# Kernel tuning notes

Hardware: AMD Instinct MI355X
Metric: run time of the kernel (lower is better)

## Reference

```python
import jax, jax.numpy as jnp
import numpy as np

HIDDEN = 1024
HEADS = 16
HEAD_DIM = HIDDEN // HEADS  # 64
LOCAL = (128, 128)
ROPE_MAX_POS = LOCAL[0] + LOCAL[1]  # 256 (local attention branch)
ROPE_BASE = 10000.0


def make_rope_cache(max_len, dim, base):
    positions = jnp.arange(max_len, dtype=jnp.float32)
    theta = 1.0 / base ** (jnp.arange(0, dim, 2, dtype=jnp.float32) / dim)
    angles = jnp.einsum('i,j->ij', positions, theta)
    return jnp.stack([jnp.cos(angles), jnp.sin(angles)], axis=-1)  # (max_len, dim//2, 2)


def apply_rope(x, cache):
    # x: (B, S, H, D); cache: (max_pos, D//2, 2)
    S = x.shape[1]
    pos = jnp.arange(S) % cache.shape[0]
    rc = cache[pos][None, :, None, :, :]  # (1, S, 1, D//2, 2)
    xr = x.reshape(*x.shape[:-1], -1, 2)
    x0, x1 = xr[..., 0], xr[..., 1]
    c, s = rc[..., 0], rc[..., 1]
    out = jnp.stack([x0 * c - x1 * s, x1 * c + x0 * s], axis=-1)
    return out.reshape(x.shape)


def sliding_window_mask(S, window, dtype):
    rel = jnp.arange(S)[:, None] - jnp.arange(S)[None, :]
    inside = (rel >= -window[0]) & (rel <= window[1])
    return jnp.where(inside, jnp.zeros((), dtype), -jnp.inf)[None, None]  # (1,1,S,S)


def setup_inputs() -> dict:
    key = jax.random.key(0)
    k1, k2, k3, k4, k5 = jax.random.split(key, 5)
    B, S = 2, 2048
    hidden_states = jax.random.normal(k1, (B, S, HIDDEN), dtype=jnp.float32)
    Wqkv_kernel = jax.random.normal(k2, (HIDDEN, 3 * HIDDEN), dtype=jnp.float32) / np.sqrt(HIDDEN)
    Wqkv_bias = jnp.zeros((3 * HIDDEN,), dtype=jnp.float32)
    Wo_kernel = jax.random.normal(k3, (HIDDEN, HIDDEN), dtype=jnp.float32) / np.sqrt(HIDDEN)
    Wo_bias = jnp.zeros((HIDDEN,), dtype=jnp.float32)
    rope_cache = make_rope_cache(ROPE_MAX_POS, HEAD_DIM, ROPE_BASE)
    return {
        'hidden_states': hidden_states,
        'Wqkv_kernel': Wqkv_kernel,
        'Wqkv_bias': Wqkv_bias,
        'Wo_kernel': Wo_kernel,
        'Wo_bias': Wo_bias,
        'rope_cache': rope_cache,
    }


def reference(hidden_states, Wqkv_kernel, Wqkv_bias, Wo_kernel, Wo_bias, rope_cache):
    B, S, _ = hidden_states.shape
    qkv = hidden_states @ Wqkv_kernel + Wqkv_bias  # (B,S,3*HIDDEN)
    qkv = qkv.reshape(B, S, 3, HEADS, HEAD_DIM)
    q = qkv[:, :, 0]  # (B,S,H,D)
    k = qkv[:, :, 1]
    v = qkv[:, :, 2]
    q = apply_rope(q, rope_cache)
    k = apply_rope(k, rope_cache)
    # to (B,H,S,D)
    q = jnp.transpose(q, (0, 2, 1, 3))
    k = jnp.transpose(k, (0, 2, 1, 3))
    v = jnp.transpose(v, (0, 2, 1, 3))
    scale = jnp.sqrt(jnp.float32(HEAD_DIM))
    scores = jnp.einsum('bhqd,bhkd->bhqk', q, k) / scale
    mask = sliding_window_mask(S, LOCAL, scores.dtype)
    probs = jax.nn.softmax(scores + mask, axis=-1)
    out = jnp.einsum('bhqk,bhkd->bqhd', probs, v).reshape(B, S, HIDDEN)
    out = out @ Wo_kernel + Wo_bias
    return out
```

## Files before the change

### kernel.cpp

```cpp
#include <hip/hip_runtime.h>
#include <hip/hip_bf16.h>

typedef __bf16 bf16x8 __attribute__((ext_vector_type(8)));
typedef __bf16 bf16x4 __attribute__((ext_vector_type(4)));
typedef float f32x4 __attribute__((ext_vector_type(4)));

#define SLEN 2048
#define NHEADS 16
#define HDIM 64

__global__ __launch_bounds__(256) void prep(const float* __restrict__ hidden,
                                            const float* __restrict__ Wqkv,
                                            const float* __restrict__ Wo,
                                            __bf16* __restrict__ A1,
                                            __bf16* __restrict__ Wt,
                                            __bf16* __restrict__ Wot) {
    int b = blockIdx.x;
    if (b < 4096) {
        int i = b * 256 + threadIdx.x;
        float4 v = reinterpret_cast<const float4*>(hidden)[i];
        bf16x4 o = { (__bf16)v.x, (__bf16)v.y, (__bf16)v.z, (__bf16)v.w };
        reinterpret_cast<bf16x4*>(A1)[i] = o;
        return;
    }
    __shared__ float tile[32][33];
    const float* W; __bf16* Dst; int N, n0, kc, bx, wn, j0, JNv;
    if (b < 7168) {
        int bb = b - 4096;
        int bx96 = bb % 96; kc = bb / 96;
        W = Wqkv; Dst = Wt; N = 3072;
        n0 = bx96 * 32;
        bx = bx96 >> 2; wn = (bx96 >> 1) & 1; j0 = (bx96 & 1) * 2; JNv = 4;
    } else {
        int bb = b - 7168;
        int bx32 = bb % 32; kc = bb / 32;
        W = Wo; Dst = Wot; N = 1024;
        n0 = bx32 * 32;
        bx = bx32 >> 1; wn = bx32 & 1; j0 = 0; JNv = 2;
    }
    int k0 = kc * 32;
    int tx = threadIdx.x & 31, ty = threadIdx.x >> 5;
    #pragma unroll
    for (int i = ty; i < 32; i += 8)
        tile[i][tx] = W[(size_t)(k0 + i) * N + n0 + tx];
    __syncthreads();
    if (threadIdx.x < 128) {
        int jh = threadIdx.x >> 6;
        int lane = threadIdx.x & 63;
        int lrow = lane & 15, quad = lane >> 4;
        bf16x8 val;
        #pragma unroll
        for (int i = 0; i < 8; i++)
            val[i] = (__bf16)tile[quad * 8 + i][jh * 16 + lrow];
        size_t idx = ((((size_t)(bx * 32 + kc) * 2 + wn) * JNv + (j0 + jh)) * 64 + lane);
        *reinterpret_cast<bf16x8*>(Dst + idx * 8) = val;
    }
}

template <int TN>
__global__ __launch_bounds__(256) void gemm_bt(const __bf16* __restrict__ A,
                                               const __bf16* __restrict__ Bfrag,
                                               const float* __restrict__ bias,
                                               float* __restrict__ Cf,
                                               __bf16* __restrict__ Cq,
                                               __bf16* __restrict__ Ck,
                                               __bf16* __restrict__ Cv,
                                               int M, int N, int K, int epi) {
    constexpr int JN = TN / 32;
    __shared__ __align__(16) __bf16 As[128 * 40];

    int nb = N / TN;
    int bx = blockIdx.x % nb;
    int by = blockIdx.x / nb;
    int row0 = by * 128, col0 = bx * TN;

    int tid = threadIdx.x;
    int wave = tid >> 6, lane = tid & 63;
    int quad = lane >> 4, lrow = lane & 15;
    int wm = wave >> 1, wn = wave & 1;

    int r1 = tid >> 2;
    int kk = (tid & 3) * 8;
    const __bf16* Aptr = A + (size_t)(row0 + r1) * K + kk;

    const __bf16* Bbase = Bfrag + ((size_t)(bx * 32) * 2 + wn) * JN * 512 + (size_t)lane * 8;

    f32x4 acc[4][JN];
    f32x4 zero = {0.f, 0.f, 0.f, 0.f};
    #pragma unroll
    for (int i = 0; i < 4; i++)
        #pragma unroll
        for (int j = 0; j < JN; j++) acc[i][j] = zero;

    int nkc = K >> 5;
    for (int kc = 0; kc < nkc; kc++) {
        int k0 = kc * 32;
        bf16x8 a0 = *reinterpret_cast<const bf16x8*>(Aptr + k0);
        bf16x8 a1 = *reinterpret_cast<const bf16x8*>(Aptr + (size_t)64 * K + k0);
        bf16x8 bfr[JN];
        #pragma unroll
        for (int j = 0; j < JN; j++)
            bfr[j] = *reinterpret_cast<const bf16x8*>(Bbase + (size_t)kc * JN * 1024 + j * 512);
        __syncthreads();
        *reinterpret_cast<bf16x8*>(&As[r1 * 40 + kk]) = a0;
        *reinterpret_cast<bf16x8*>(&As[(r1 + 64) * 40 + kk]) = a1;
        __syncthreads();

        bf16x8 af[4];
        #pragma unroll
        for (int i = 0; i < 4; i++)
            af[i] = *reinterpret_cast<const bf16x8*>(&As[(wm * 64 + i * 16 + lrow) * 40 + quad * 8]);
        #pragma unroll
        for (int i = 0; i < 4; i++)
            #pragma unroll
            for (int j = 0; j < JN; j++)
                acc[i][j] = __builtin_amdgcn_mfma_f32_16x16x32_bf16(af[i], bfr[j], acc[i][j], 0, 0, 0);
    }

    int part = col0 >> 10;
    #pragma unroll
    for (int i = 0; i < 4; i++) {
        int rowb = row0 + wm * 64 + i * 16 + quad * 4;
        #pragma unroll
        for (int j = 0; j < JN; j++) {
            int col = col0 + wn * (TN / 2) + j * 16 + lrow;
            float bsv = bias[col];
            #pragma unroll
            for (int r = 0; r < 4; r++) {
                int row = rowb + r;
                float v = acc[i][j][r] + bsv;
                if (epi == 0) {
                    Cf[(size_t)row * N + col] = v;
                } else {
                    int h = (col >> 6) & 15;
                    int d = col & 63;
                    int b = row >> 11;
                    int s = row & 2047;
                    __bf16* dst = (part == 0) ? Cq : ((part == 1) ? Ck : Cv);
                    dst[((size_t)(b * NHEADS + h) * SLEN + s) * HDIM + d] = (__bf16)v;
                }
            }
        }
    }
}

__device__ __forceinline__ bf16x8 rope8(bf16x8 v, f32x4 a, f32x4 b) {
    bf16x8 o;
    float e, od;
    e = (float)v[0]; od = (float)v[1];
    o[0] = (__bf16)(e * a[0] - od * a[1]); o[1] = (__bf16)(od * a[0] + e * a[1]);
    e = (float)v[2]; od = (float)v[3];
    o[2] = (__bf16)(e * a[2] - od * a[3]); o[3] = (__bf16)(od * a[2] + e * a[3]);
    e = (float)v[4]; od = (float)v[5];
    o[4] = (__bf16)(e * b[0] - od * b[1]); o[5] = (__bf16)(od * b[0] + e * b[1]);
    e = (float)v[6]; od = (float)v[7];
    o[6] = (__bf16)(e * b[2] - od * b[3]); o[7] = (__bf16)(od * b[2] + e * b[3]);
    return o;
}

__global__ __launch_bounds__(256) void rope_kernel(__bf16* __restrict__ Q,
                                                   __bf16* __restrict__ K,
                                                   const float* __restrict__ rope) {
    int idx = blockIdx.x * 256 + threadIdx.x;
    int chunk = idx & 7;
    int s = (idx >> 3) & 2047;
    int bh = idx >> 14;
    size_t off = ((size_t)bh * SLEN + s) * HDIM + chunk * 8;
    int pos = s & 255;
    const float* rp = rope + (size_t)pos * 64 + chunk * 8;
    f32x4 a = *reinterpret_cast<const f32x4*>(rp);
    f32x4 b = *reinterpret_cast<const f32x4*>(rp + 4);
    bf16x8 qv = *reinterpret_cast<bf16x8*>(Q + off);
    *reinterpret_cast<bf16x8*>(Q + off) = rope8(qv, a, b);
    bf16x8 kv = *reinterpret_cast<bf16x8*>(K + off);
    *reinterpret_cast<bf16x8*>(K + off) = rope8(kv, a, b);
}

__global__ __launch_bounds__(256) void attn_kernel(const __bf16* __restrict__ Q,
                                                   const __bf16* __restrict__ K,
                                                   const __bf16* __restrict__ V,
                                                   __bf16* __restrict__ O) {
    __shared__ __align__(16) __bf16 Vt[64][328];
    __shared__ __align__(16) __bf16 Pl[4][16][80];

    int qt = blockIdx.x & 31;
    int bh = blockIdx.x >> 5;
    int q0 = qt * 64;
    int kbase0 = q0 - 128;
    const __bf16* Qbh = Q + (size_t)bh * SLEN * HDIM;
    const __bf16* Kbh = K + (size_t)bh * SLEN * HDIM;
    const __bf16* Vbh = V + (size_t)bh * SLEN * HDIM;

    int tid = threadIdx.x;
    int wave = tid >> 6, lane = tid & 63;
    int quad = lane >> 4, lrow = lane & 15;
    int wq0 = q0 + wave * 16;

    {
        int dchunk = wave * 16;
        #pragma unroll
        for (int k = 0; k < 5; k++) {
            int off = k * 64 + lane;
            int krow = kbase0 + off;
            krow = min(max(krow, 0), SLEN - 1);
            const __bf16* vp = Vbh + (size_t)krow * HDIM + dchunk;
            bf16x8 v0 = *reinterpret_cast<const bf16x8*>(vp);
            bf16x8 v1 = *reinterpret_cast<const bf16x8*>(vp + 8);
            #pragma unroll
            for (int i = 0; i < 8; i++) {
                Vt[dchunk + i][off] = v0[i];
                Vt[dchunk + 8 + i][off] = v1[i];
            }
        }
    }

    bf16x8 qb0 = *reinterpret_cast<const bf16x8*>(Qbh + (size_t)(wq0 + lrow) * HDIM + quad * 8);
    bf16x8 qb1 = *reinterpret_cast<const bf16x8*>(Qbh + (size_t)(wq0 + lrow) * HDIM + 32 + quad * 8);

    __syncthreads();

    f32x4 zero = {0.f, 0.f, 0.f, 0.f};
    f32x4 acc[4], acc_l = zero;
    #pragma unroll
    for (int t = 0; t < 4; t++) acc[t] = zero;

    bf16x8 ones = { (__bf16)1.f, (__bf16)1.f, (__bf16)1.f, (__bf16)1.f,
                    (__bf16)1.f, (__bf16)1.f, (__bf16)1.f, (__bf16)1.f };

    int cbeg = wave >> 1;
    if (q0 < 128) { int e = (128 - q0) >> 5; if (e > cbeg) cbeg = e; }
    int cend = (16 * wave + 271) >> 5;
    { int e = (2175 - q0) >> 5; if (e < cend) cend = e; }

    auto loadK = [&](int c, bf16x8 (&kf)[2][2]) {
        int kb = kbase0 + c * 32;
        #pragma unroll
        for (int sub = 0; sub < 2; sub++) {
            int kr = kb + sub * 16 + lrow;
            int krc = min(max(kr, 0), SLEN - 1);
            const __bf16* kp = Kbh + (size_t)krc * HDIM;
            kf[sub][0] = *reinterpret_cast<const bf16x8*>(kp + quad * 8);
            kf[sub][1] = *reinterpret_cast<const bf16x8*>(kp + 32 + quad * 8);
        }
    };

    auto qkExp = [&](int c, bf16x8 (&kf)[2][2], int slot) {
        int kb = kbase0 + c * 32;
        int q = wq0 + lrow;
        #pragma unroll
        for (int sub = 0; sub < 2; sub++) {
            f32x4 st = __builtin_amdgcn_mfma_f32_16x16x32_bf16(kf[sub][0], qb0, zero, 0, 0, 0);
            st = __builtin_amdgcn_mfma_f32_16x16x32_bf16(kf[sub][1], qb1, st, 0, 0, 0);
            bf16x4 pk;
            #pragma unroll
            for (int r = 0; r < 4; r++) {
                int key = kb + sub * 16 + quad * 4 + r;
                int rel = key - q;
                bool valid = (rel >= -128) && (rel <= 128) && (key >= 0) && (key < SLEN);
                pk[r] = (__bf16)(valid ? __expf(st[r] * 0.125f) : 0.0f);
            }
            *reinterpret_cast<bf16x4*>(&Pl[wave][lrow][slot * 40 + sub * 16 + quad * 4]) = pk;
        }
    };

    auto pv = [&](int c, int slot) {
        int loc = c * 32;
        bf16x8 bp = *reinterpret_cast<const bf16x8*>(&Pl[wave][lrow][slot * 40 + quad * 8]);
        acc_l = __builtin_amdgcn_mfma_f32_16x16x32_bf16(ones, bp, acc_l, 0, 0, 0);
        #pragma unroll
        for (int t = 0; t < 4; t++) {
            bf16x8 va = *reinterpret_cast<const bf16x8*>(&Vt[t * 16 + lrow][loc + quad * 8]);
            acc[t] = __builtin_amdgcn_mfma_f32_16x16x32_bf16(va, bp, acc[t], 0, 0, 0);
        }
    };

    bf16x8 ka0[2][2], ka1[2][2];
    loadK(cbeg, ka0);
    loadK(cbeg + 1, ka1);
    int c = cbeg;
    while (c + 1 <= cend) {
        bf16x8 kn0[2][2], kn1[2][2];
        loadK(c + 2, kn0);
        loadK(c + 3, kn1);
        qkExp(c, ka0, 0);
        qkExp(c + 1, ka1, 1);
        asm volatile("s_waitcnt lgkmcnt(0)" ::: "memory");
        pv(c, 0);
        pv(c + 1, 1);
        #pragma unroll
        for (int sub = 0; sub < 2; sub++) {
            ka0[sub][0] = kn0[sub][0]; ka0[sub][1] = kn0[sub][1];
            ka1[sub][0] = kn1[sub][0]; ka1[sub][1] = kn1[sub][1];
        }
        c += 2;
    }
    if (c <= cend) {
        qkExp(c, ka0, 0);
        asm volatile("s_waitcnt lgkmcnt(0)" ::: "memory");
        pv(c, 0);
    }

    float inv = 1.0f / acc_l[0];
    int b = bh >> 4, h = bh & 15;
    int q = wq0 + lrow;
    size_t base = ((size_t)b * SLEN + q) * 1024 + h * HDIM;
    #pragma unroll
    for (int t = 0; t < 4; t++) {
        bf16x4 o;
        #pragma unroll
        for (int r = 0; r < 4; r++) o[r] = (__bf16)(acc[t][r] * inv);
        *reinterpret_cast<bf16x4*>(&O[base + t * 16 + quad * 4]) = o;
    }
}

extern "C" void kernel_launch(void* const* d_in, const int* in_sizes, int n_in,
                              void* d_out, int out_size, void* d_ws, size_t ws_size,
                              hipStream_t stream) {
    const float* hidden = (const float*)d_in[0];
    const float* Wqkv   = (const float*)d_in[1];
    const float* bqkv   = (const float*)d_in[2];
    const float* Wo     = (const float*)d_in[3];
    const float* bo     = (const float*)d_in[4];
    const float* rope   = (const float*)d_in[5];
    float* out = (float*)d_out;

    char* ws = (char*)d_ws;
    __bf16* A1  = (__bf16*)(ws);
    __bf16* Wt  = (__bf16*)(ws + 8388608);
    __bf16* Wot = (__bf16*)(ws + 14680064);
    __bf16* Qb  = (__bf16*)(ws + 16777216);
    __bf16* Kb  = (__bf16*)(ws + 25165824);
    __bf16* Vb  = (__bf16*)(ws + 33554432);
    __bf16* AO  = (__bf16*)(ws + 41943040);

    prep<<<8192, 256, 0, stream>>>(hidden, Wqkv, Wo, A1, Wt, Wot);

    gemm_bt<128><<<32 * 24, 256, 0, stream>>>(A1, Wt, bqkv, nullptr, Qb, Kb, Vb,
                                              4096, 3072, 1024, 1);
    rope_kernel<<<2048, 256, 0, stream>>>(Qb, Kb, rope);
    attn_kernel<<<1024, 256, 0, stream>>>(Qb, Kb, Vb, AO);
    gemm_bt<64><<<32 * 16, 256, 0, stream>>>(AO, Wot, bo, out, nullptr, nullptr, nullptr,
                                             4096, 1024, 1024, 0);
}
```

Before: 182.1 us.

## Pre-swizzle activations into MFMA fragment layout and use LDS-free QKV GEMM

```diff
diff --git a/kernel.cpp b/kernel.cpp
--- a/kernel.cpp
+++ b/kernel.cpp
@@ -16,37 +16,59 @@
                                             __bf16* __restrict__ Wt,
                                             __bf16* __restrict__ Wot) {
     int b = blockIdx.x;
-    if (b < 4096) {
-        int i = b * 256 + threadIdx.x;
-        float4 v = reinterpret_cast<const float4*>(hidden)[i];
-        bf16x4 o = { (__bf16)v.x, (__bf16)v.y, (__bf16)v.z, (__bf16)v.w };
-        reinterpret_cast<bf16x4*>(A1)[i] = o;
+    int t = threadIdx.x;
+    if (b < 1024) {
+        __shared__ float tile[128][33];
+        int by = b >> 5, kc = b & 31;
+        const float* src = hidden + (size_t)(by * 128) * 1024 + kc * 32;
+        #pragma unroll
+        for (int it = 0; it < 4; it++) {
+            int linear = it * 256 + t;
+            int r = linear >> 3, c4 = (linear & 7) * 4;
+            float4 v = *reinterpret_cast<const float4*>(src + (size_t)r * 1024 + c4);
+            tile[r][c4] = v.x; tile[r][c4 + 1] = v.y;
+            tile[r][c4 + 2] = v.z; tile[r][c4 + 3] = v.w;
+        }
+        __syncthreads();
+        int lane = t & 63, g = t >> 6;
+        int lrow = lane & 15, quad = lane >> 4;
+        #pragma unroll
+        for (int h = 0; h < 2; h++) {
+            int gg = g + h * 4;
+            int wm = gg >> 2, i = gg & 3;
+            int r = wm * 64 + i * 16 + lrow, c = quad * 8;
+            bf16x8 val;
+            #pragma unroll
+            for (int e = 0; e < 8; e++) val[e] = (__bf16)tile[r][c + e];
+            size_t off = ((size_t)by * 32 + kc) * 4096 + wm * 2048 + (size_t)i * 512 + (size_t)lane * 8;
+            *reinterpret_cast<bf16x8*>(A1 + off) = val;
+        }
         return;
     }
     __shared__ float tile[32][33];
     const float* W; __bf16* Dst; int N, n0, kc, bx, wn, j0, JNv;
-    if (b < 7168) {
-        int bb = b - 4096;
+    if (b < 4096) {
+        int bb = b - 1024;
         int bx96 = bb % 96; kc = bb / 96;
         W = Wqkv; Dst = Wt; N = 3072;
         n0 = bx96 * 32;
         bx = bx96 >> 2; wn = (bx96 >> 1) & 1; j0 = (bx96 & 1) * 2; JNv = 4;
     } else {
-        int bb = b - 7168;
+        int bb = b - 4096;
         int bx32 = bb % 32; kc = bb / 32;
         W = Wo; Dst = Wot; N = 1024;
         n0 = bx32 * 32;
         bx = bx32 >> 1; wn = bx32 & 1; j0 = 0; JNv = 2;
     }
     int k0 = kc * 32;
-    int tx = threadIdx.x & 31, ty = threadIdx.x >> 5;
+    int tx = t & 31, ty = t >> 5;
     #pragma unroll
     for (int i = ty; i < 32; i += 8)
         tile[i][tx] = W[(size_t)(k0 + i) * N + n0 + tx];
     __syncthreads();
-    if (threadIdx.x < 128) {
-        int jh = threadIdx.x >> 6;
-        int lane = threadIdx.x & 63;
+    if (t < 128) {
+        int jh = t >> 6;
+        int lane = t & 63;
         int lrow = lane & 15, quad = lane >> 4;
         bf16x8 val;
         #pragma unroll
@@ -54,6 +76,89 @@
             val[i] = (__bf16)tile[quad * 8 + i][jh * 16 + lrow];
         size_t idx = ((((size_t)(bx * 32 + kc) * 2 + wn) * JNv + (j0 + jh)) * 64 + lane);
         *reinterpret_cast<bf16x8*>(Dst + idx * 8) = val;
+    }
+}
+
+__global__ __launch_bounds__(256) void gemm_qkv(const __bf16* __restrict__ Af,
+                                                const __bf16* __restrict__ Bf,
+                                                const float* __restrict__ bias,
+                                                __bf16* __restrict__ Cq,
+                                                __bf16* __restrict__ Ck,
+                                                __bf16* __restrict__ Cv) {
+    int bx = blockIdx.x % 24;
+    int by = blockIdx.x / 24;
+    int row0 = by * 128, col0 = bx * 128;
+
+    int tid = threadIdx.x;
+    int wave = tid >> 6, lane = tid & 63;
+    int quad = lane >> 4, lrow = lane & 15;
+    int wm = wave >> 1, wn = wave & 1;
+
+    const __bf16* Abase = Af + (size_t)by * 131072 + wm * 2048 + (size_t)lane * 8;
+    const __bf16* Bbase = Bf + (size_t)bx * 131072 + wn * 2048 + (size_t)lane * 8;
+
+    f32x4 acc[4][4];
+    f32x4 zero = {0.f, 0.f, 0.f, 0.f};
+    #pragma unroll
+    for (int i = 0; i < 4; i++)
+        #pragma unroll
+        for (int j = 0; j < 4; j++) acc[i][j] = zero;
+
+    bf16x8 a0[4], b0[4], a1[4], b1[4];
+    #pragma unroll
+    for (int i = 0; i < 4; i++) {
+        a0[i] = *reinterpret_cast<const bf16x8*>(Abase + i * 512);
+        b0[i] = *reinterpret_cast<const bf16x8*>(Bbase + i * 512);
+    }
+
+    #pragma unroll 1
+    for (int kc = 0; kc < 32; kc += 2) {
+        size_t o1 = (size_t)(kc + 1) * 4096;
+        #pragma unroll
+        for (int i = 0; i < 4; i++) {
+            a1[i] = *reinterpret_cast<const bf16x8*>(Abase + o1 + i * 512);
+            b1[i] = *reinterpret_cast<const bf16x8*>(Bbase + o1 + i * 512);
+        }
+        #pragma unroll
+        for (int i = 0; i < 4; i++)
+            #pragma unroll
+            for (int j = 0; j < 4; j++)
+                acc[i][j] = __builtin_amdgcn_mfma_f32_16x16x32_bf16(a0[i], b0[j], acc[i][j], 0, 0, 0);
+        if (kc + 2 < 32) {
+            size_t o2 = (size_t)(kc + 2) * 4096;
+            #pragma unroll
+            for (int i = 0; i < 4; i++) {
+                a0[i] = *reinterpret_cast<const bf16x8*>(Abase + o2 + i * 512);
+                b0[i] = *reinterpret_cast<const bf16x8*>(Bbase + o2 + i * 512);
+            }
+        }
+        #pragma unroll
+        for (int i = 0; i < 4; i++)
+            #pragma unroll
+            for (int j = 0; j < 4; j++)
+                acc[i][j] = __builtin_amdgcn_mfma_f32_16x16x32_bf16(a1[i], b1[j], acc[i][j], 0, 0, 0);
+    }
+
+    int part = col0 >> 10;
+    #pragma unroll
+    for (int i = 0; i < 4; i++) {
+        int rowb = row0 + wm * 64 + i * 16 + quad * 4;
+        #pragma unroll
+        for (int j = 0; j < 4; j++) {
+            int col = col0 + wn * 64 + j * 16 + lrow;
+            float bsv = bias[col];
+            #pragma unroll
+            for (int r = 0; r < 4; r++) {
+                int row = rowb + r;
+                float v = acc[i][j][r] + bsv;
+                int h = (col >> 6) & 15;
+                int d = col & 63;
+                int b = row >> 11;
+                int s = row & 2047;
+                __bf16* dst = (part == 0) ? Cq : ((part == 1) ? Ck : Cv);
+                dst[((size_t)(b * NHEADS + h) * SLEN + s) * HDIM + d] = (__bf16)v;
+            }
+        }
     }
 }
 
@@ -62,10 +167,7 @@
                                                const __bf16* __restrict__ Bfrag,
                                                const float* __restrict__ bias,
                                                float* __restrict__ Cf,
-                                               __bf16* __restrict__ Cq,
-                                               __bf16* __restrict__ Ck,
-                                               __bf16* __restrict__ Cv,
-                                               int M, int N, int K, int epi) {
+                                               int M, int N, int K) {
     constexpr int JN = TN / 32;
     __shared__ __align__(16) __bf16 As[128 * 40];
 
@@ -117,7 +219,6 @@
                 acc[i][j] = __builtin_amdgcn_mfma_f32_16x16x32_bf16(af[i], bfr[j], acc[i][j], 0, 0, 0);
     }
 
-    int part = col0 >> 10;
     #pragma unroll
     for (int i = 0; i < 4; i++) {
         int rowb = row0 + wm * 64 + i * 16 + quad * 4;
@@ -128,17 +229,7 @@
             #pragma unroll
             for (int r = 0; r < 4; r++) {
                 int row = rowb + r;
-                float v = acc[i][j][r] + bsv;
-                if (epi == 0) {
-                    Cf[(size_t)row * N + col] = v;
-                } else {
-                    int h = (col >> 6) & 15;
-                    int d = col & 63;
-                    int b = row >> 11;
-                    int s = row & 2047;
-                    __bf16* dst = (part == 0) ? Cq : ((part == 1) ? Ck : Cv);
-                    dst[((size_t)(b * NHEADS + h) * SLEN + s) * HDIM + d] = (__bf16)v;
-                }
+                Cf[(size_t)row * N + col] = acc[i][j][r] + bsv;
             }
         }
     }
@@ -333,12 +424,10 @@
     __bf16* Vb  = (__bf16*)(ws + 33554432);
     __bf16* AO  = (__bf16*)(ws + 41943040);
 
-    prep<<<8192, 256, 0, stream>>>(hidden, Wqkv, Wo, A1, Wt, Wot);
-
-    gemm_bt<128><<<32 * 24, 256, 0, stream>>>(A1, Wt, bqkv, nullptr, Qb, Kb, Vb,
-                                              4096, 3072, 1024, 1);
+    prep<<<5120, 256, 0, stream>>>(hidden, Wqkv, Wo, A1, Wt, Wot);
+
+    gemm_qkv<<<32 * 24, 256, 0, stream>>>(A1, Wt, bqkv, Qb, Kb, Vb);
     rope_kernel<<<2048, 256, 0, stream>>>(Qb, Kb, rope);
     attn_kernel<<<1024, 256, 0, stream>>>(Qb, Kb, Vb, AO);
-    gemm_bt<64><<<32 * 16, 256, 0, stream>>>(AO, Wot, bo, out, nullptr, nullptr, nullptr,
-                                             4096, 1024, 1024, 0);
-}
+    gemm_bt<64><<<32 * 16, 256, 0, stream>>>(AO, Wot, bo, out, 4096, 1024, 1024);
+}
```

Measured after the change: 189.7 us. 4.2% more time.

## Write V transposed from QKV GEMM epilogue and stream V fragments from global

Applied to the files above, without the earlier changes.

```diff
diff --git a/kernel.cpp b/kernel.cpp
--- a/kernel.cpp
+++ b/kernel.cpp
@@ -125,19 +125,25 @@
         for (int j = 0; j < JN; j++) {
             int col = col0 + wn * (TN / 2) + j * 16 + lrow;
             float bsv = bias[col];
-            #pragma unroll
-            for (int r = 0; r < 4; r++) {
-                int row = rowb + r;
-                float v = acc[i][j][r] + bsv;
-                if (epi == 0) {
-                    Cf[(size_t)row * N + col] = v;
+            if (epi == 0) {
+                #pragma unroll
+                for (int r = 0; r < 4; r++)
+                    Cf[(size_t)(rowb + r) * N + col] = acc[i][j][r] + bsv;
+            } else {
+                int h = (col >> 6) & 15;
+                int d = col & 63;
+                int b = rowb >> 11;
+                int s0 = rowb & 2047;
+                if (part == 2) {
+                    bf16x4 vv;
+                    #pragma unroll
+                    for (int r = 0; r < 4; r++) vv[r] = (__bf16)(acc[i][j][r] + bsv);
+                    *reinterpret_cast<bf16x4*>(Cv + ((size_t)(b * NHEADS + h) * HDIM + d) * SLEN + s0) = vv;
                 } else {
-                    int h = (col >> 6) & 15;
-                    int d = col & 63;
-                    int b = row >> 11;
-                    int s = row & 2047;
-                    __bf16* dst = (part == 0) ? Cq : ((part == 1) ? Ck : Cv);
-                    dst[((size_t)(b * NHEADS + h) * SLEN + s) * HDIM + d] = (__bf16)v;
+                    __bf16* dst = (part == 0) ? Cq : Ck;
+                    #pragma unroll
+                    for (int r = 0; r < 4; r++)
+                        dst[((size_t)(b * NHEADS + h) * SLEN + s0 + r) * HDIM + d] = (__bf16)(acc[i][j][r] + bsv);
                 }
             }
         }
@@ -178,9 +184,8 @@
 
 __global__ __launch_bounds__(256) void attn_kernel(const __bf16* __restrict__ Q,
                                                    const __bf16* __restrict__ K,
-                                                   const __bf16* __restrict__ V,
+                                                   const __bf16* __restrict__ Vt,
                                                    __bf16* __restrict__ O) {
-    __shared__ __align__(16) __bf16 Vt[64][328];
     __shared__ __align__(16) __bf16 Pl[4][16][80];
 
     int qt = blockIdx.x & 31;
@@ -189,35 +194,15 @@
     int kbase0 = q0 - 128;
     const __bf16* Qbh = Q + (size_t)bh * SLEN * HDIM;
     const __bf16* Kbh = K + (size_t)bh * SLEN * HDIM;
-    const __bf16* Vbh = V + (size_t)bh * SLEN * HDIM;
+    const __bf16* Vbh = Vt + (size_t)bh * SLEN * HDIM;
 
     int tid = threadIdx.x;
     int wave = tid >> 6, lane = tid & 63;
     int quad = lane >> 4, lrow = lane & 15;
     int wq0 = q0 + wave * 16;
 
-    {
-        int dchunk = wave * 16;
-        #pragma unroll
-        for (int k = 0; k < 5; k++) {
-            int off = k * 64 + lane;
-            int krow = kbase0 + off;
-            krow = min(max(krow, 0), SLEN - 1);
-            const __bf16* vp = Vbh + (size_t)krow * HDIM + dchunk;
-            bf16x8 v0 = *reinterpret_cast<const bf16x8*>(vp);
-            bf16x8 v1 = *reinterpret_cast<const bf16x8*>(vp + 8);
-            #pragma unroll
-            for (int i = 0; i < 8; i++) {
-                Vt[dchunk + i][off] = v0[i];
-                Vt[dchunk + 8 + i][off] = v1[i];
-            }
-        }
-    }
-
     bf16x8 qb0 = *reinterpret_cast<const bf16x8*>(Qbh + (size_t)(wq0 + lrow) * HDIM + quad * 8);
     bf16x8 qb1 = *reinterpret_cast<const bf16x8*>(Qbh + (size_t)(wq0 + lrow) * HDIM + 32 + quad * 8);
-
-    __syncthreads();
 
     f32x4 zero = {0.f, 0.f, 0.f, 0.f};
     f32x4 acc[4], acc_l = zero;
@@ -243,6 +228,13 @@
             kf[sub][1] = *reinterpret_cast<const bf16x8*>(kp + 32 + quad * 8);
         }
     };
+    auto loadV = [&](int c, bf16x8 (&vf)[4]) {
+        int col = kbase0 + c * 32;
+        col = min(max(col, 0), SLEN - 32);
+        #pragma unroll
+        for (int t = 0; t < 4; t++)
+            vf[t] = *reinterpret_cast<const bf16x8*>(Vbh + (size_t)(t * 16 + lrow) * SLEN + col + quad * 8);
+    };
 
     auto qkExp = [&](int c, bf16x8 (&kf)[2][2], int slot) {
         int kb = kbase0 + c * 32;
@@ -256,48 +248,47 @@
             for (int r = 0; r < 4; r++) {
                 int key = kb + sub * 16 + quad * 4 + r;
                 int rel = key - q;
-                bool valid = (rel >= -128) && (rel <= 128) && (key >= 0) && (key < SLEN);
+                bool valid = (rel >= -128) && (rel <= 128);
                 pk[r] = (__bf16)(valid ? __expf(st[r] * 0.125f) : 0.0f);
             }
             *reinterpret_cast<bf16x4*>(&Pl[wave][lrow][slot * 40 + sub * 16 + quad * 4]) = pk;
         }
     };
 
-    auto pv = [&](int c, int slot) {
-        int loc = c * 32;
+    auto pv = [&](bf16x8 (&vf)[4], int slot) {
         bf16x8 bp = *reinterpret_cast<const bf16x8*>(&Pl[wave][lrow][slot * 40 + quad * 8]);
         acc_l = __builtin_amdgcn_mfma_f32_16x16x32_bf16(ones, bp, acc_l, 0, 0, 0);
         #pragma unroll
-        for (int t = 0; t < 4; t++) {
-            bf16x8 va = *reinterpret_cast<const bf16x8*>(&Vt[t * 16 + lrow][loc + quad * 8]);
-            acc[t] = __builtin_amdgcn_mfma_f32_16x16x32_bf16(va, bp, acc[t], 0, 0, 0);
-        }
+        for (int t = 0; t < 4; t++)
+            acc[t] = __builtin_amdgcn_mfma_f32_16x16x32_bf16(vf[t], bp, acc[t], 0, 0, 0);
     };
 
-    bf16x8 ka0[2][2], ka1[2][2];
-    loadK(cbeg, ka0);
-    loadK(cbeg + 1, ka1);
+    bf16x8 ka0[2][2], ka1[2][2], va0[4], va1[4];
+    loadK(cbeg, ka0); loadV(cbeg, va0);
+    loadK(cbeg + 1, ka1); loadV(cbeg + 1, va1);
     int c = cbeg;
     while (c + 1 <= cend) {
-        bf16x8 kn0[2][2], kn1[2][2];
-        loadK(c + 2, kn0);
-        loadK(c + 3, kn1);
+        bf16x8 kn0[2][2], kn1[2][2], vn0[4], vn1[4];
+        loadK(c + 2, kn0); loadV(c + 2, vn0);
+        loadK(c + 3, kn1); loadV(c + 3, vn1);
         qkExp(c, ka0, 0);
         qkExp(c + 1, ka1, 1);
         asm volatile("s_waitcnt lgkmcnt(0)" ::: "memory");
-        pv(c, 0);
-        pv(c + 1, 1);
+        pv(va0, 0);
+        pv(va1, 1);
         #pragma unroll
         for (int sub = 0; sub < 2; sub++) {
             ka0[sub][0] = kn0[sub][0]; ka0[sub][1] = kn0[sub][1];
             ka1[sub][0] = kn1[sub][0]; ka1[sub][1] = kn1[sub][1];
         }
+        #pragma unroll
+        for (int t = 0; t < 4; t++) { va0[t] = vn0[t]; va1[t] = vn1[t]; }
         c += 2;
     }
     if (c <= cend) {
         qkExp(c, ka0, 0);
         asm volatile("s_waitcnt lgkmcnt(0)" ::: "memory");
-        pv(c, 0);
+        pv(va0, 0);
     }
 
     float inv = 1.0f / acc_l[0];
```

Result: slower. 191.7 us (+5.3%).

## Double-buffer A tile in LDS and prefetch next K-chunk in GEMM

Applied to the files above, without the earlier changes.

```diff
diff --git a/kernel.cpp b/kernel.cpp
--- a/kernel.cpp
+++ b/kernel.cpp
@@ -67,7 +67,7 @@
                                                __bf16* __restrict__ Cv,
                                                int M, int N, int K, int epi) {
     constexpr int JN = TN / 32;
-    __shared__ __align__(16) __bf16 As[128 * 40];
+    __shared__ __align__(16) __bf16 As[2][128 * 40];
 
     int nb = N / TN;
     int bx = blockIdx.x % nb;
@@ -93,28 +93,49 @@
         for (int j = 0; j < JN; j++) acc[i][j] = zero;
 
     int nkc = K >> 5;
+
+    {
+        bf16x8 a0 = *reinterpret_cast<const bf16x8*>(Aptr);
+        bf16x8 a1 = *reinterpret_cast<const bf16x8*>(Aptr + (size_t)64 * K);
+        *reinterpret_cast<bf16x8*>(&As[0][r1 * 40 + kk]) = a0;
+        *reinterpret_cast<bf16x8*>(&As[0][(r1 + 64) * 40 + kk]) = a1;
+    }
+    bf16x8 bR[JN];
+    #pragma unroll
+    for (int j = 0; j < JN; j++)
+        bR[j] = *reinterpret_cast<const bf16x8*>(Bbase + j * 512);
+    __syncthreads();
+
     for (int kc = 0; kc < nkc; kc++) {
-        int k0 = kc * 32;
-        bf16x8 a0 = *reinterpret_cast<const bf16x8*>(Aptr + k0);
-        bf16x8 a1 = *reinterpret_cast<const bf16x8*>(Aptr + (size_t)64 * K + k0);
-        bf16x8 bfr[JN];
-        #pragma unroll
-        for (int j = 0; j < JN; j++)
-            bfr[j] = *reinterpret_cast<const bf16x8*>(Bbase + (size_t)kc * JN * 1024 + j * 512);
-        __syncthreads();
-        *reinterpret_cast<bf16x8*>(&As[r1 * 40 + kk]) = a0;
-        *reinterpret_cast<bf16x8*>(&As[(r1 + 64) * 40 + kk]) = a1;
-        __syncthreads();
+        int p = kc & 1;
+        bool more = (kc + 1) < nkc;
+        bf16x8 aN0, aN1, bN[JN];
+        if (more) {
+            int k0 = (kc + 1) * 32;
+            aN0 = *reinterpret_cast<const bf16x8*>(Aptr + k0);
+            aN1 = *reinterpret_cast<const bf16x8*>(Aptr + (size_t)64 * K + k0);
+            #pragma unroll
+            for (int j = 0; j < JN; j++)
+                bN[j] = *reinterpret_cast<const bf16x8*>(Bbase + (size_t)(kc + 1) * JN * 1024 + j * 512);
+        }
 
         bf16x8 af[4];
         #pragma unroll
         for (int i = 0; i < 4; i++)
-            af[i] = *reinterpret_cast<const bf16x8*>(&As[(wm * 64 + i * 16 + lrow) * 40 + quad * 8]);
+            af[i] = *reinterpret_cast<const bf16x8*>(&As[p][(wm * 64 + i * 16 + lrow) * 40 + quad * 8]);
         #pragma unroll
         for (int i = 0; i < 4; i++)
             #pragma unroll
             for (int j = 0; j < JN; j++)
-                acc[i][j] = __builtin_amdgcn_mfma_f32_16x16x32_bf16(af[i], bfr[j], acc[i][j], 0, 0, 0);
+                acc[i][j] = __builtin_amdgcn_mfma_f32_16x16x32_bf16(af[i], bR[j], acc[i][j], 0, 0, 0);
+
+        if (more) {
+            *reinterpret_cast<bf16x8*>(&As[p ^ 1][r1 * 40 + kk]) = aN0;
+            *reinterpret_cast<bf16x8*>(&As[p ^ 1][(r1 + 64) * 40 + kk]) = aN1;
+            __syncthreads();
+            #pragma unroll
+            for (int j = 0; j < JN; j++) bR[j] = bN[j];
+        }
     }
 
     int part = col0 >> 10;
```

New measurement: 179.3 us. No clear change (-1.5%).
